# Performance work log

Hardware: AMD Instinct MI355X
Metric: run time of the kernel (lower is better)

Reference implementation:

```python
import jax, jax.numpy as jnp
import numpy as np

D_MODEL = 1024
NUM_HEADS = 16
D_K = D_MODEL // NUM_HEADS
SCALE = D_K ** 0.5


def setup_inputs() -> dict:
    key = jax.random.key(0)
    k1, k2, k3, k4, k5 = jax.random.split(key, 5)
    B, T = 4, 2048
    x = jax.random.normal(k1, (B, T, D_MODEL), dtype=jnp.float32)
    # torch nn.Linear: y = x @ W.T + b ; store W in (in, out) layout for jax
    s = 1.0 / np.sqrt(D_MODEL)
    w_qkv = jax.random.uniform(k2, (D_MODEL, 3 * D_MODEL), jnp.float32, -s, s)
    b_qkv = jax.random.uniform(k3, (3 * D_MODEL,), jnp.float32, -s, s)
    w_out = jax.random.uniform(k4, (D_MODEL, D_MODEL), jnp.float32, -s, s)
    b_out = jax.random.uniform(k5, (D_MODEL,), jnp.float32, -s, s)
    return {"x": x, "w_qkv": w_qkv, "b_qkv": b_qkv, "w_out": w_out, "b_out": b_out}


def reference(x, w_qkv, b_qkv, w_out, b_out):
    B, T, D = x.shape
    qkv = x @ w_qkv + b_qkv  # (B, T, 3D)
    q, k, v = jnp.split(qkv, 3, axis=-1)

    def split_heads(t):
        return t.reshape(B, T, NUM_HEADS, D_K).transpose(0, 2, 1, 3)  # (B,H,T,d_k)

    q, k, v = split_heads(q), split_heads(k), split_heads(v)
    scores = jnp.einsum("bhtd,bhsd->bhts", q, k) / SCALE  # (B,H,T,T)
    attn = jax.nn.softmax(scores, axis=-1)
    ctx = jnp.einsum("bhts,bhsd->bhtd", attn, v)  # (B,H,T,d_k)
    ctx = ctx.transpose(0, 2, 1, 3).reshape(B, T, D)
    y = ctx @ w_out + b_out
    return y
```

## Files before the change

### kernel.cpp

```cpp
#include <hip/hip_runtime.h>
#include <hip/hip_bf16.h>


using v8bf  = __attribute__((ext_vector_type(8))) __bf16;
using f32x4 = __attribute__((ext_vector_type(4))) float;
using f32x16 = __attribute__((ext_vector_type(16))) float;
typedef unsigned int uv2 __attribute__((ext_vector_type(2)));

__device__ __forceinline__ unsigned short f2bf(float f) {
  union { float f; unsigned int u; } v; v.f = f;
  unsigned int u = v.u;
  u += 0x7FFFu + ((u >> 16) & 1u);
  return (unsigned short)(u >> 16);
}

#if __has_builtin(__builtin_amdgcn_cvt_pk_bf16_f32)
__device__ __forceinline__ unsigned int pack2bf(float a, float b) {
  typedef __bf16 bf16x2 __attribute__((ext_vector_type(2)));
  bf16x2 r = __builtin_amdgcn_cvt_pk_bf16_f32(a, b);
  return __builtin_bit_cast(unsigned int, r);
}
#else
__device__ __forceinline__ unsigned int pack2bf(float a, float b) {
  return (unsigned int)f2bf(a) | ((unsigned int)f2bf(b) << 16);
}
#endif

__device__ __forceinline__ void async16(const void* g, void* l) {
  __builtin_amdgcn_global_load_lds(
      (__attribute__((address_space(1))) void*)g,
      (__attribute__((address_space(3))) void*)l, 16, 0, 0);
}

__global__ __launch_bounds__(256) void convert_bf16(const float* __restrict__ in,
                                                    unsigned short* __restrict__ out,
                                                    int n) {
  int i = (blockIdx.x * 256 + threadIdx.x) * 4;
  if (i < n) {
    float4 v = *(const float4*)(in + i);
    ushort4 o;
    o.x = f2bf(v.x); o.y = f2bf(v.y); o.z = f2bf(v.z); o.w = f2bf(v.w);
    *(ushort4*)(out + i) = o;
  }
}

__global__ __launch_bounds__(256) void transpose_bf16(const float* __restrict__ in,
                                                      unsigned short* __restrict__ out,
                                                      int K, int N) {
  __shared__ unsigned short tile[64][65];
  int k0 = blockIdx.x * 64, n0 = blockIdx.y * 64;
  for (int i = threadIdx.x; i < 4096; i += 256) {
    int r = i >> 6, c = i & 63;
    tile[r][c] = f2bf(in[(size_t)(k0 + r) * N + n0 + c]);
  }
  __syncthreads();
  for (int i = threadIdx.x; i < 4096; i += 256) {
    int r = i >> 6, c = i & 63;
    out[(size_t)(n0 + r) * K + k0 + c] = tile[c][r];
  }
}

__device__ __forceinline__ void gemm128(const unsigned short* __restrict__ A,
                                        const unsigned short* __restrict__ Bt,
                                        int m0, int n0,
                                        unsigned short* As, unsigned short* Bs,
                                        f32x4 acc[4][4]) {
  const int tid = threadIdx.x;
  const int w = tid >> 6, lane = tid & 63, quad = lane >> 4, l16 = lane & 15;
  const int wm = (w >> 1) * 64, wn = (w & 1) * 64;

  const int srow = w * 32 + (lane >> 3);
  const int cg = (lane & 7) ^ (lane >> 3);
  const size_t a_g = (size_t)(m0 + srow) * 1024 + cg * 8;
  const size_t b_g = (size_t)(n0 + srow) * 1024 + cg * 8;
  const int lds_off = srow * 64 + (lane & 7) * 8;

  const int l7 = l16 & 7;
  const int a_rd0 = (wm + l16) * 128 + ((quad ^ l7) << 4);
  const int a_rd1 = (wm + l16) * 128 + (((4 + quad) ^ l7) << 4);
  const int b_rd0 = (wn + l16) * 128 + ((quad ^ l7) << 4);
  const int b_rd1 = (wn + l16) * 128 + (((4 + quad) ^ l7) << 4);

  for (int k0 = 0; k0 < 1024; k0 += 64) {
#pragma unroll
    for (int j = 0; j < 4; j++) {
      async16(A + a_g + (size_t)j * 8192 + k0, As + lds_off + j * 512);
      async16(Bt + b_g + (size_t)j * 8192 + k0, Bs + lds_off + j * 512);
    }
    __syncthreads();
#pragma unroll
    for (int ks = 0; ks < 2; ks++) {
      v8bf af[4], bfr[4];
#pragma unroll
      for (int i = 0; i < 4; i++) {
        af[i]  = *(const v8bf*)((const char*)As + (ks ? a_rd1 : a_rd0) + i * 2048);
        bfr[i] = *(const v8bf*)((const char*)Bs + (ks ? b_rd1 : b_rd0) + i * 2048);
      }
#pragma unroll
      for (int i = 0; i < 4; i++)
#pragma unroll
        for (int jn = 0; jn < 4; jn++)
          acc[i][jn] = __builtin_amdgcn_mfma_f32_16x16x32_bf16(af[i], bfr[jn], acc[i][jn], 0, 0, 0);
    }
    __syncthreads();
  }
}

__global__ __launch_bounds__(256) void qkv_gemm(const unsigned short* __restrict__ xb,
                                                const unsigned short* __restrict__ wt,
                                                const float* __restrict__ bias,
                                                unsigned short* __restrict__ Q,
                                                unsigned short* __restrict__ K,
                                                unsigned short* __restrict__ VT) {
  __shared__ __align__(16) unsigned char pool[128 * 136 * 2];
  unsigned short* As = (unsigned short*)pool;
  unsigned short* Bs = (unsigned short*)(pool + 16384);
  unsigned short* Tr = (unsigned short*)pool;

  f32x4 acc[4][4];
#pragma unroll
  for (int i = 0; i < 4; i++)
#pragma unroll
    for (int j = 0; j < 4; j++) acc[i][j] = (f32x4){0.f, 0.f, 0.f, 0.f};

  const int m0 = blockIdx.x * 128, n0 = blockIdx.y * 128;
  gemm128(xb, wt, m0, n0, As, Bs, acc);

  const int tid = threadIdx.x;
  const int w = tid >> 6, lane = tid & 63, quad = lane >> 4, l16 = lane & 15;
  const int wm = (w >> 1) * 64, wn = (w & 1) * 64;
  const int seg = n0 >> 10;

  if (seg < 2) {
    const float sc = (seg == 0) ? 0.18033688011112042f : 1.0f;
    unsigned short* dst = (seg == 0) ? Q : K;
#pragma unroll
    for (int jn = 0; jn < 4; jn++) {
      const int n = n0 + wn + jn * 16 + l16;
      const float bv = bias[n];
      const int nn = n & 1023, h = nn >> 6, d = nn & 63;
#pragma unroll
      for (int i = 0; i < 4; i++) {
#pragma unroll
        for (int r = 0; r < 4; r++) {
          const int m = m0 + wm + i * 16 + quad * 4 + r;
          const int b_ = m >> 11, t = m & 2047;
          dst[(((size_t)(b_ * 16 + h)) * 2048 + t) * 64 + d] =
              f2bf((acc[i][jn][r] + bv) * sc);
        }
      }
    }
  } else {
    const int TP = 136;
#pragma unroll
    for (int jn = 0; jn < 4; jn++) {
      const int nl = wn + jn * 16 + l16;
      const float bv = bias[n0 + nl];
#pragma unroll
      for (int i = 0; i < 4; i++) {
        const int ml = wm + i * 16 + quad * 4;
        ushort4 v4;
        v4.x = f2bf(acc[i][jn][0] + bv);
        v4.y = f2bf(acc[i][jn][1] + bv);
        v4.z = f2bf(acc[i][jn][2] + bv);
        v4.w = f2bf(acc[i][jn][3] + bv);
        *(ushort4*)&Tr[nl * TP + ml] = v4;
      }
    }
    __syncthreads();
    const int rl = tid >> 1, cb = (tid & 1) * 64;
    const int h0 = (n0 & 1023) >> 6;
    const int h = h0 + (rl >> 6), d = rl & 63;
    const int b_ = m0 >> 11, t = m0 & 2047;
    unsigned short* dst = VT + (((size_t)(b_ * 16 + h)) * 64 + d) * 2048 + t + cb;
    const unsigned short* src = &Tr[rl * TP + cb];
#pragma unroll
    for (int c = 0; c < 8; c++)
      *(uint4*)(dst + c * 8) = *(const uint4*)(src + c * 8);
  }
}

__global__ __launch_bounds__(256, 2) void flash_attn(const unsigned short* __restrict__ Q,
                                                     const unsigned short* __restrict__ K,
                                                     const unsigned short* __restrict__ VT,
                                                     unsigned short* __restrict__ ctx) {
  const int bh    = blockIdx.x;
  const int qtile = blockIdx.y;
  const int tid = threadIdx.x;
  const int w = tid >> 6, lane = tid & 63, hi = lane >> 5, l32 = lane & 31;
  const int q0 = qtile * 256;

  const unsigned short* Qb = Q  + (size_t)bh * 2048 * 64;
  const unsigned short* Kb = K  + (size_t)bh * 2048 * 64;
  const unsigned short* Vb = VT + (size_t)bh * 64 * 2048;

  __shared__ __align__(16) unsigned short Ks[3 * 4096];
  __shared__ __align__(16) unsigned short Vs[3 * 4096];

  const int sr = w * 8 + (lane >> 3);
  const int cg = (lane & 7) ^ ((lane >> 3) & 7);
  const int lds_off = sr * 64 + (lane & 7) * 8;

  v8bf qf[2][4];
#pragma unroll
  for (int qt = 0; qt < 2; qt++) {
    const int qrow = q0 + w * 64 + qt * 32 + l32;
#pragma unroll
    for (int kc = 0; kc < 4; kc++)
      qf[qt][kc] = *(const v8bf*)(Qb + (size_t)qrow * 64 + kc * 16 + hi * 8);
  }

  f32x16 o[2][2];
  f32x16 st[2][2];
  float l_[2] = {0.f, 0.f};
#pragma unroll
  for (int qt = 0; qt < 2; qt++)
#pragma unroll
    for (int mt = 0; mt < 2; mt++)
#pragma unroll
      for (int r = 0; r < 16; r++) o[qt][mt][r] = 0.f;

  f32x16 fz;
#pragma unroll
  for (int r = 0; r < 16; r++) fz[r] = 0.f;

  auto stage = [&](int buf, int s0) {
    unsigned short* Kd = Ks + buf * 4096;
    unsigned short* Vd = Vs + buf * 4096;
#pragma unroll
    for (int j = 0; j < 2; j++) {
      async16(Kb + (size_t)(s0 + sr + j * 32) * 64 + cg * 8, Kd + lds_off + j * 2048);
      async16(Vb + (size_t)(sr + j * 32) * 2048 + s0 + cg * 8, Vd + lds_off + j * 2048);
    }
  };

  const int l7 = l32 & 7;

  auto computeS = [&](const unsigned short* Kc) {
#pragma unroll
    for (int sf = 0; sf < 2; sf++) {
      v8bf ak[4];
#pragma unroll
      for (int kc = 0; kc < 4; kc++)
        ak[kc] = *(const v8bf*)((const char*)Kc +
                   (sf * 32 + l32) * 128 + (((2 * kc + hi) ^ l7) << 4));
#pragma unroll
      for (int qt = 0; qt < 2; qt++) {
        f32x16 s = __builtin_amdgcn_mfma_f32_32x32x16_bf16(ak[0], qf[qt][0], fz, 0, 0, 0);
#pragma unroll
        for (int kc = 1; kc < 4; kc++)
          s = __builtin_amdgcn_mfma_f32_32x32x16_bf16(ak[kc], qf[qt][kc], s, 0, 0, 0);
        st[qt][sf] = s;
      }
    }
  };

  auto softmax_pack = [&](uint2 pk[2][2][4]) {
#pragma unroll
    for (int qt = 0; qt < 2; qt++) {
      float a = 0.f;
#pragma unroll
      for (int sf = 0; sf < 2; sf++)
#pragma unroll
        for (int r = 0; r < 16; r++) {
          const float pv = __builtin_amdgcn_exp2f(st[qt][sf][r]);
          st[qt][sf][r] = pv;
          a += pv;
        }
      l_[qt] += a;
#pragma unroll
      for (int sf = 0; sf < 2; sf++)
#pragma unroll
        for (int g = 0; g < 4; g++) {
          pk[qt][sf][g].x = pack2bf(st[qt][sf][g * 4 + 0], st[qt][sf][g * 4 + 1]);
          pk[qt][sf][g].y = pack2bf(st[qt][sf][g * 4 + 2], st[qt][sf][g * 4 + 3]);
        }
    }
  };

  auto pv = [&](const unsigned short* Vc, uint2 pk[2][2][4]) {
    v8bf vf[2][4];
#pragma unroll
    for (int mt = 0; mt < 2; mt++)
#pragma unroll
      for (int kc = 0; kc < 4; kc++)
        vf[mt][kc] = *(const v8bf*)((const char*)Vc +
                       (mt * 32 + l32) * 128 + (((2 * kc + hi) ^ l7) << 4));
#pragma unroll
    for (int qt = 0; qt < 2; qt++) {
#pragma unroll
      for (int kc = 0; kc < 4; kc++) {
        const int sf = kc >> 1, c2 = (kc & 1) * 2;
        const uint2 olo = pk[qt][sf][c2];
        const uint2 ohi = pk[qt][sf][c2 + 1];
        uint4 u;
#if __has_builtin(__builtin_amdgcn_permlane32_swap)
        uv2 rx = __builtin_amdgcn_permlane32_swap(olo.x, ohi.x, false, false);
        uv2 ry = __builtin_amdgcn_permlane32_swap(olo.y, ohi.y, false, false);
        u.x = rx[0]; u.y = ry[0]; u.z = rx[1]; u.w = ry[1];
#else
        uint2 send, recv;
        send.x = hi ? olo.x : ohi.x;
        send.y = hi ? olo.y : ohi.y;
        recv.x = __shfl_xor(send.x, 32, 64);
        recv.y = __shfl_xor(send.y, 32, 64);
        u.x = hi ? recv.x : olo.x;
        u.y = hi ? recv.y : olo.y;
        u.z = hi ? ohi.x : recv.x;
        u.w = hi ? ohi.y : recv.y;
#endif
        const v8bf pf = __builtin_bit_cast(v8bf, u);
#pragma unroll
        for (int mt = 0; mt < 2; mt++)
          o[qt][mt] = __builtin_amdgcn_mfma_f32_32x32x16_bf16(vf[mt][kc], pf, o[qt][mt], 0, 0, 0);
      }
    }
  };

  stage(0, 0);
  __syncthreads();
  stage(1, 64);
  computeS(Ks);

  int cs = 1, cp = 0, cn = 2;
  for (int it = 1; it < 32; ++it) {
    __syncthreads();
    if (it < 31) stage(cn, (it + 1) * 64);
    uint2 pk[2][2][4];
    softmax_pack(pk);
    computeS(Ks + cs * 4096);
    pv(Vs + cp * 4096, pk);
    const int t = cp; cp = cs; cs = cn; cn = t;
  }
  {
    uint2 pk[2][2][4];
    softmax_pack(pk);
    pv(Vs + cp * 4096, pk);
  }

  const int b_ = bh >> 4, h = bh & 15;
#pragma unroll
  for (int qt = 0; qt < 2; qt++) {
    float lt = l_[qt];
    lt += __shfl_xor(lt, 32, 64);
    const float inv = 1.0f / lt;
    const int t = q0 + w * 64 + qt * 32 + l32;
    unsigned short* cr = ctx + ((size_t)(b_ * 2048 + t)) * 1024 + h * 64;
#pragma unroll
    for (int mt = 0; mt < 2; mt++)
#pragma unroll
      for (int g = 0; g < 4; g++) {
        uint2 pkv;
        pkv.x = pack2bf(o[qt][mt][g * 4 + 0] * inv, o[qt][mt][g * 4 + 1] * inv);
        pkv.y = pack2bf(o[qt][mt][g * 4 + 2] * inv, o[qt][mt][g * 4 + 3] * inv);
        *(uint2*)(cr + mt * 32 + g * 8 + hi * 4) = pkv;
      }
  }
}

__global__ __launch_bounds__(256) void out_gemm(const unsigned short* __restrict__ ctx,
                                                const unsigned short* __restrict__ wt,
                                                const float* __restrict__ bias,
                                                float* __restrict__ out) {
  __shared__ __align__(16) unsigned short As[128 * 64];
  __shared__ __align__(16) unsigned short Bs[128 * 64];
  f32x4 acc[4][4];
#pragma unroll
  for (int i = 0; i < 4; i++)
#pragma unroll
    for (int j = 0; j < 4; j++) acc[i][j] = (f32x4){0.f, 0.f, 0.f, 0.f};

  const int m0 = blockIdx.x * 128, n0 = blockIdx.y * 128;
  gemm128(ctx, wt, m0, n0, As, Bs, acc);

  const int tid = threadIdx.x;
  const int w = tid >> 6, lane = tid & 63, quad = lane >> 4, l16 = lane & 15;
  const int wm = (w >> 1) * 64, wn = (w & 1) * 64;
#pragma unroll
  for (int jn = 0; jn < 4; jn++) {
    const int n = n0 + wn + jn * 16 + l16;
    const float bv = bias[n];
#pragma unroll
    for (int i = 0; i < 4; i++) {
#pragma unroll
      for (int r = 0; r < 4; r++) {
        const int m = m0 + wm + i * 16 + quad * 4 + r;
        out[(size_t)m * 1024 + n] = acc[i][jn][r] + bv;
      }
    }
  }
}

extern "C" void kernel_launch(void* const* d_in, const int* in_sizes, int n_in,
                              void* d_out, int out_size, void* d_ws, size_t ws_size,
                              hipStream_t stream) {
  const float* x     = (const float*)d_in[0];
  const float* w_qkv = (const float*)d_in[1];
  const float* b_qkv = (const float*)d_in[2];
  const float* w_out = (const float*)d_in[3];
  const float* b_out = (const float*)d_in[4];
  float* out = (float*)d_out;

  char* ws = (char*)d_ws;
  unsigned short* XB  = (unsigned short*)(ws + 0);
  unsigned short* WQT = (unsigned short*)(ws + 16777216);
  unsigned short* WOT = (unsigned short*)(ws + 23068672);
  unsigned short* Qp  = (unsigned short*)(ws + 25165824);
  unsigned short* Kp  = (unsigned short*)(ws + 41943040);
  unsigned short* VTp = (unsigned short*)(ws + 58720256);
  unsigned short* CTX = (unsigned short*)(ws + 75497472);

  convert_bf16<<<8192, 256, 0, stream>>>(x, XB, 8388608);
  transpose_bf16<<<dim3(16, 48), 256, 0, stream>>>(w_qkv, WQT, 1024, 3072);
  transpose_bf16<<<dim3(16, 16), 256, 0, stream>>>(w_out, WOT, 1024, 1024);
  qkv_gemm<<<dim3(64, 24), 256, 0, stream>>>(XB, WQT, b_qkv, Qp, Kp, VTp);
  flash_attn<<<dim3(64, 8), 256, 0, stream>>>(Qp, Kp, VTp, CTX);
  out_gemm<<<dim3(64, 8), 256, 0, stream>>>(CTX, WOT, b_out, out);
}
```

Measured before the change: 265.6 us.

## Halve flash-attention query tile per block to raise occupancy and block count

Each wave now handles 32 query rows instead of 64, so each block covers 128 queries and twice as many blocks are launched. Register arrays for the accumulators and scores are halved, and the launch bound is raised to 4 blocks per CU. K staging drops to double buffering while V keeps three buffers. The loop now runs PV before the next S computation, and V fragments are loaded from LDS inside the PV loop. The cost is that every K/V tile is reloaded from memory twice as often, since less reuse happens per block.

```diff
diff --git a/kernel.cpp b/kernel.cpp
--- a/kernel.cpp
+++ b/kernel.cpp
@@ -180,7 +180,7 @@
   }
 }
 
-__global__ __launch_bounds__(256, 2) void flash_attn(const unsigned short* __restrict__ Q,
+__global__ __launch_bounds__(256, 4) void flash_attn(const unsigned short* __restrict__ Q,
                                                      const unsigned short* __restrict__ K,
                                                      const unsigned short* __restrict__ VT,
                                                      unsigned short* __restrict__ ctx) {
@@ -188,50 +188,46 @@
   const int qtile = blockIdx.y;
   const int tid = threadIdx.x;
   const int w = tid >> 6, lane = tid & 63, hi = lane >> 5, l32 = lane & 31;
-  const int q0 = qtile * 256;
+  const int q0 = qtile * 128;
 
   const unsigned short* Qb = Q  + (size_t)bh * 2048 * 64;
   const unsigned short* Kb = K  + (size_t)bh * 2048 * 64;
   const unsigned short* Vb = VT + (size_t)bh * 64 * 2048;
 
-  __shared__ __align__(16) unsigned short Ks[3 * 4096];
+  __shared__ __align__(16) unsigned short Ks[2 * 4096];
   __shared__ __align__(16) unsigned short Vs[3 * 4096];
 
   const int sr = w * 8 + (lane >> 3);
   const int cg = (lane & 7) ^ ((lane >> 3) & 7);
   const int lds_off = sr * 64 + (lane & 7) * 8;
 
-  v8bf qf[2][4];
-#pragma unroll
-  for (int qt = 0; qt < 2; qt++) {
-    const int qrow = q0 + w * 64 + qt * 32 + l32;
+  v8bf qf[4];
+  {
+    const int qrow = q0 + w * 32 + l32;
 #pragma unroll
     for (int kc = 0; kc < 4; kc++)
-      qf[qt][kc] = *(const v8bf*)(Qb + (size_t)qrow * 64 + kc * 16 + hi * 8);
-  }
-
-  f32x16 o[2][2];
-  f32x16 st[2][2];
-  float l_[2] = {0.f, 0.f};
-#pragma unroll
-  for (int qt = 0; qt < 2; qt++)
-#pragma unroll
-    for (int mt = 0; mt < 2; mt++)
-#pragma unroll
-      for (int r = 0; r < 16; r++) o[qt][mt][r] = 0.f;
-
-  f32x16 fz;
-#pragma unroll
-  for (int r = 0; r < 16; r++) fz[r] = 0.f;
-
-  auto stage = [&](int buf, int s0) {
+      qf[kc] = *(const v8bf*)(Qb + (size_t)qrow * 64 + kc * 16 + hi * 8);
+  }
+
+  f32x16 o[2];
+  f32x16 st[2];
+  float l_ = 0.f;
+#pragma unroll
+  for (int mt = 0; mt < 2; mt++)
+#pragma unroll
+    for (int r = 0; r < 16; r++) o[mt][r] = 0.f;
+
+  auto stageK = [&](int buf, int s0) {
     unsigned short* Kd = Ks + buf * 4096;
+#pragma unroll
+    for (int j = 0; j < 2; j++)
+      async16(Kb + (size_t)(s0 + sr + j * 32) * 64 + cg * 8, Kd + lds_off + j * 2048);
+  };
+  auto stageV = [&](int buf, int s0) {
     unsigned short* Vd = Vs + buf * 4096;
 #pragma unroll
-    for (int j = 0; j < 2; j++) {
-      async16(Kb + (size_t)(s0 + sr + j * 32) * 64 + cg * 8, Kd + lds_off + j * 2048);
+    for (int j = 0; j < 2; j++)
       async16(Vb + (size_t)(sr + j * 32) * 2048 + s0 + cg * 8, Vd + lds_off + j * 2048);
-    }
   };
 
   const int l7 = l32 & 7;
@@ -244,115 +240,94 @@
       for (int kc = 0; kc < 4; kc++)
         ak[kc] = *(const v8bf*)((const char*)Kc +
                    (sf * 32 + l32) * 128 + (((2 * kc + hi) ^ l7) << 4));
-#pragma unroll
-      for (int qt = 0; qt < 2; qt++) {
-        f32x16 s = __builtin_amdgcn_mfma_f32_32x32x16_bf16(ak[0], qf[qt][0], fz, 0, 0, 0);
-#pragma unroll
-        for (int kc = 1; kc < 4; kc++)
-          s = __builtin_amdgcn_mfma_f32_32x32x16_bf16(ak[kc], qf[qt][kc], s, 0, 0, 0);
-        st[qt][sf] = s;
-      }
-    }
-  };
-
-  auto softmax_pack = [&](uint2 pk[2][2][4]) {
-#pragma unroll
-    for (int qt = 0; qt < 2; qt++) {
-      float a = 0.f;
-#pragma unroll
-      for (int sf = 0; sf < 2; sf++)
-#pragma unroll
-        for (int r = 0; r < 16; r++) {
-          const float pv = __builtin_amdgcn_exp2f(st[qt][sf][r]);
-          st[qt][sf][r] = pv;
-          a += pv;
-        }
-      l_[qt] += a;
-#pragma unroll
-      for (int sf = 0; sf < 2; sf++)
-#pragma unroll
-        for (int g = 0; g < 4; g++) {
-          pk[qt][sf][g].x = pack2bf(st[qt][sf][g * 4 + 0], st[qt][sf][g * 4 + 1]);
-          pk[qt][sf][g].y = pack2bf(st[qt][sf][g * 4 + 2], st[qt][sf][g * 4 + 3]);
-        }
-    }
-  };
-
-  auto pv = [&](const unsigned short* Vc, uint2 pk[2][2][4]) {
-    v8bf vf[2][4];
-#pragma unroll
-    for (int mt = 0; mt < 2; mt++)
-#pragma unroll
-      for (int kc = 0; kc < 4; kc++)
-        vf[mt][kc] = *(const v8bf*)((const char*)Vc +
-                       (mt * 32 + l32) * 128 + (((2 * kc + hi) ^ l7) << 4));
-#pragma unroll
-    for (int qt = 0; qt < 2; qt++) {
-#pragma unroll
-      for (int kc = 0; kc < 4; kc++) {
-        const int sf = kc >> 1, c2 = (kc & 1) * 2;
-        const uint2 olo = pk[qt][sf][c2];
-        const uint2 ohi = pk[qt][sf][c2 + 1];
-        uint4 u;
+      f32x16 s = __builtin_amdgcn_mfma_f32_32x32x16_bf16(ak[0], qf[0], (f32x16)(0.f), 0, 0, 0);
+#pragma unroll
+      for (int kc = 1; kc < 4; kc++)
+        s = __builtin_amdgcn_mfma_f32_32x32x16_bf16(ak[kc], qf[kc], s, 0, 0, 0);
+      st[sf] = s;
+    }
+  };
+
+  auto softmax = [&]() {
+    float a0 = 0.f, a1 = 0.f;
+#pragma unroll
+    for (int sf = 0; sf < 2; sf++)
+#pragma unroll
+      for (int r = 0; r < 16; r++) {
+        const float pv = __builtin_amdgcn_exp2f(st[sf][r]);
+        st[sf][r] = pv;
+        if (r & 1) a1 += pv; else a0 += pv;
+      }
+    l_ += a0 + a1;
+  };
+
+  auto pv = [&](const unsigned short* Vc) {
+#pragma unroll
+    for (int kc = 0; kc < 4; kc++) {
+      const int sf = kc >> 1, e0 = (kc & 1) * 8;
+      uint2 olo, ohi;
+      olo.x = pack2bf(st[sf][e0 + 0], st[sf][e0 + 1]);
+      olo.y = pack2bf(st[sf][e0 + 2], st[sf][e0 + 3]);
+      ohi.x = pack2bf(st[sf][e0 + 4], st[sf][e0 + 5]);
+      ohi.y = pack2bf(st[sf][e0 + 6], st[sf][e0 + 7]);
+      uint4 u;
 #if __has_builtin(__builtin_amdgcn_permlane32_swap)
-        uv2 rx = __builtin_amdgcn_permlane32_swap(olo.x, ohi.x, false, false);
-        uv2 ry = __builtin_amdgcn_permlane32_swap(olo.y, ohi.y, false, false);
-        u.x = rx[0]; u.y = ry[0]; u.z = rx[1]; u.w = ry[1];
+      uv2 rx = __builtin_amdgcn_permlane32_swap(olo.x, ohi.x, false, false);
+      uv2 ry = __builtin_amdgcn_permlane32_swap(olo.y, ohi.y, false, false);
+      u.x = rx[0]; u.y = ry[0]; u.z = rx[1]; u.w = ry[1];
 #else
-        uint2 send, recv;
-        send.x = hi ? olo.x : ohi.x;
-        send.y = hi ? olo.y : ohi.y;
-        recv.x = __shfl_xor(send.x, 32, 64);
-        recv.y = __shfl_xor(send.y, 32, 64);
-        u.x = hi ? recv.x : olo.x;
-        u.y = hi ? recv.y : olo.y;
-        u.z = hi ? ohi.x : recv.x;
-        u.w = hi ? ohi.y : recv.y;
+      uint2 send, recv;
+      send.x = hi ? olo.x : ohi.x;
+      send.y = hi ? olo.y : ohi.y;
+      recv.x = __shfl_xor(send.x, 32, 64);
+      recv.y = __shfl_xor(send.y, 32, 64);
+      u.x = hi ? recv.x : olo.x;
+      u.y = hi ? recv.y : olo.y;
+      u.z = hi ? ohi.x : recv.x;
+      u.w = hi ? ohi.y : recv.y;
 #endif
-        const v8bf pf = __builtin_bit_cast(v8bf, u);
-#pragma unroll
-        for (int mt = 0; mt < 2; mt++)
-          o[qt][mt] = __builtin_amdgcn_mfma_f32_32x32x16_bf16(vf[mt][kc], pf, o[qt][mt], 0, 0, 0);
-      }
-    }
-  };
-
-  stage(0, 0);
+      const v8bf pf = __builtin_bit_cast(v8bf, u);
+#pragma unroll
+      for (int mt = 0; mt < 2; mt++) {
+        const v8bf vfm = *(const v8bf*)((const char*)Vc +
+                           (mt * 32 + l32) * 128 + (((2 * kc + hi) ^ l7) << 4));
+        o[mt] = __builtin_amdgcn_mfma_f32_32x32x16_bf16(vfm, pf, o[mt], 0, 0, 0);
+      }
+    }
+  };
+
+  stageK(0, 0); stageV(0, 0);
   __syncthreads();
-  stage(1, 64);
+  stageK(1, 64); stageV(1, 64);
   computeS(Ks);
 
-  int cs = 1, cp = 0, cn = 2;
+  int vp = 0, vn = 2;
   for (int it = 1; it < 32; ++it) {
     __syncthreads();
-    if (it < 31) stage(cn, (it + 1) * 64);
-    uint2 pk[2][2][4];
-    softmax_pack(pk);
-    computeS(Ks + cs * 4096);
-    pv(Vs + cp * 4096, pk);
-    const int t = cp; cp = cs; cs = cn; cn = t;
-  }
+    if (it < 31) { stageK((it + 1) & 1, (it + 1) * 64); stageV(vn, (it + 1) * 64); }
+    softmax();
+    pv(Vs + vp * 4096);
+    computeS(Ks + (it & 1) * 4096);
+    vp = (vp == 2) ? 0 : vp + 1;
+    vn = (vn == 2) ? 0 : vn + 1;
+  }
+  softmax();
+  pv(Vs + vp * 4096);
+
+  const int b_ = bh >> 4, h = bh & 15;
   {
-    uint2 pk[2][2][4];
-    softmax_pack(pk);
-    pv(Vs + cp * 4096, pk);
-  }
-
-  const int b_ = bh >> 4, h = bh & 15;
-#pragma unroll
-  for (int qt = 0; qt < 2; qt++) {
-    float lt = l_[qt];
+    float lt = l_;
     lt += __shfl_xor(lt, 32, 64);
     const float inv = 1.0f / lt;
-    const int t = q0 + w * 64 + qt * 32 + l32;
+    const int t = q0 + w * 32 + l32;
     unsigned short* cr = ctx + ((size_t)(b_ * 2048 + t)) * 1024 + h * 64;
 #pragma unroll
     for (int mt = 0; mt < 2; mt++)
 #pragma unroll
       for (int g = 0; g < 4; g++) {
         uint2 pkv;
-        pkv.x = pack2bf(o[qt][mt][g * 4 + 0] * inv, o[qt][mt][g * 4 + 1] * inv);
-        pkv.y = pack2bf(o[qt][mt][g * 4 + 2] * inv, o[qt][mt][g * 4 + 3] * inv);
+        pkv.x = pack2bf(o[mt][g * 4 + 0] * inv, o[mt][g * 4 + 1] * inv);
+        pkv.y = pack2bf(o[mt][g * 4 + 2] * inv, o[mt][g * 4 + 3] * inv);
         *(uint2*)(cr + mt * 32 + g * 8 + hi * 4) = pkv;
       }
   }
@@ -414,6 +389,6 @@
   transpose_bf16<<<dim3(16, 48), 256, 0, stream>>>(w_qkv, WQT, 1024, 3072);
   transpose_bf16<<<dim3(16, 16), 256, 0, stream>>>(w_out, WOT, 1024, 1024);
   qkv_gemm<<<dim3(64, 24), 256, 0, stream>>>(XB, WQT, b_qkv, Qp, Kp, VTp);
-  flash_attn<<<dim3(64, 8), 256, 0, stream>>>(Qp, Kp, VTp, CTX);
+  flash_attn<<<dim3(64, 16), 256, 0, stream>>>(Qp, Kp, VTp, CTX);
   out_gemm<<<dim3(64, 8), 256, 0, stream>>>(CTX, WOT, b_out, out);
 }
```

After: 276.5 us. 4.1% more time.

## Use 256x128 triple-buffered pipelined GEMM tiles with block swizzle for projections

Applied to the files above, without the earlier changes.

Replaces the single-buffered 128x128 GEMM core with a 256x128 tile over 512 threads. Global-to-LDS async copies now run through a three-stage ring, gated by explicit vmcnt waits, so the next tiles load while MFMAs execute. The loop also adds s_setprio around the MFMA bursts and remaps block indices so blocks sharing a weight column-tile run close together for L2 reuse. The cost is about 144KB of LDS per block, which limits each CU to one resident block. The hand-written wait counts and barriers must also stay in step with the number of copies each stage issues.

```diff
diff --git a/kernel.cpp b/kernel.cpp
--- a/kernel.cpp
+++ b/kernel.cpp
@@ -60,7 +60,43 @@
   }
 }
 
-__device__ __forceinline__ void gemm128(const unsigned short* __restrict__ A,
+#define GKSTEP(VMSTR, CUR, DOSTAGE, KNEXT)                                     \
+  {                                                                            \
+    asm volatile("s_waitcnt vmcnt(" VMSTR ")" ::: "memory");                   \
+    __builtin_amdgcn_s_barrier();                                              \
+    __builtin_amdgcn_sched_barrier(0);                                         \
+    const unsigned short* Ab = As + (CUR) * 16384;                             \
+    const unsigned short* Bb = Bs + (CUR) * 8192;                              \
+    v8bf a0[4], b0[4], a1[4], b1[4];                                           \
+    _Pragma("unroll") for (int i_ = 0; i_ < 4; i_++) {                         \
+      a0[i_] = *(const v8bf*)((const char*)Ab + (wm + i_ * 16 + l16) * 128 +   \
+                              ((quad ^ l7) << 4));                             \
+      b0[i_] = *(const v8bf*)((const char*)Bb + (wn + i_ * 16 + l16) * 128 +   \
+                              ((quad ^ l7) << 4));                             \
+      a1[i_] = *(const v8bf*)((const char*)Ab + (wm + i_ * 16 + l16) * 128 +   \
+                              (((4 + quad) ^ l7) << 4));                       \
+      b1[i_] = *(const v8bf*)((const char*)Bb + (wn + i_ * 16 + l16) * 128 +   \
+                              (((4 + quad) ^ l7) << 4));                       \
+    }                                                                          \
+    __builtin_amdgcn_s_setprio(1);                                             \
+    _Pragma("unroll") for (int i_ = 0; i_ < 4; i_++)                           \
+      _Pragma("unroll") for (int j_ = 0; j_ < 4; j_++)                         \
+        acc[i_][j_] = __builtin_amdgcn_mfma_f32_16x16x32_bf16(                 \
+            a0[i_], b0[j_], acc[i_][j_], 0, 0, 0);                             \
+    __builtin_amdgcn_s_setprio(0);                                             \
+    asm volatile("s_waitcnt lgkmcnt(0)" ::: "memory");                         \
+    __builtin_amdgcn_s_barrier();                                              \
+    __builtin_amdgcn_sched_barrier(0);                                         \
+    if (DOSTAGE) stage((CUR), (KNEXT));                                        \
+    __builtin_amdgcn_s_setprio(1);                                             \
+    _Pragma("unroll") for (int i_ = 0; i_ < 4; i_++)                           \
+      _Pragma("unroll") for (int j_ = 0; j_ < 4; j_++)                         \
+        acc[i_][j_] = __builtin_amdgcn_mfma_f32_16x16x32_bf16(                 \
+            a1[i_], b1[j_], acc[i_][j_], 0, 0, 0);                             \
+    __builtin_amdgcn_s_setprio(0);                                             \
+  }
+
+__device__ __forceinline__ void gemm256(const unsigned short* __restrict__ A,
                                         const unsigned short* __restrict__ Bt,
                                         int m0, int n0,
                                         unsigned short* As, unsigned short* Bs,
@@ -68,53 +104,46 @@
   const int tid = threadIdx.x;
   const int w = tid >> 6, lane = tid & 63, quad = lane >> 4, l16 = lane & 15;
   const int wm = (w >> 1) * 64, wn = (w & 1) * 64;
-
-  const int srow = w * 32 + (lane >> 3);
-  const int cg = (lane & 7) ^ (lane >> 3);
-  const size_t a_g = (size_t)(m0 + srow) * 1024 + cg * 8;
-  const size_t b_g = (size_t)(n0 + srow) * 1024 + cg * 8;
-  const int lds_off = srow * 64 + (lane & 7) * 8;
-
   const int l7 = l16 & 7;
-  const int a_rd0 = (wm + l16) * 128 + ((quad ^ l7) << 4);
-  const int a_rd1 = (wm + l16) * 128 + (((4 + quad) ^ l7) << 4);
-  const int b_rd0 = (wn + l16) * 128 + ((quad ^ l7) << 4);
-  const int b_rd1 = (wn + l16) * 128 + (((4 + quad) ^ l7) << 4);
-
-  for (int k0 = 0; k0 < 1024; k0 += 64) {
-#pragma unroll
-    for (int j = 0; j < 4; j++) {
-      async16(A + a_g + (size_t)j * 8192 + k0, As + lds_off + j * 512);
-      async16(Bt + b_g + (size_t)j * 8192 + k0, Bs + lds_off + j * 512);
-    }
-    __syncthreads();
-#pragma unroll
-    for (int ks = 0; ks < 2; ks++) {
-      v8bf af[4], bfr[4];
-#pragma unroll
-      for (int i = 0; i < 4; i++) {
-        af[i]  = *(const v8bf*)((const char*)As + (ks ? a_rd1 : a_rd0) + i * 2048);
-        bfr[i] = *(const v8bf*)((const char*)Bs + (ks ? b_rd1 : b_rd0) + i * 2048);
-      }
-#pragma unroll
-      for (int i = 0; i < 4; i++)
-#pragma unroll
-        for (int jn = 0; jn < 4; jn++)
-          acc[i][jn] = __builtin_amdgcn_mfma_f32_16x16x32_bf16(af[i], bfr[jn], acc[i][jn], 0, 0, 0);
-    }
-    __syncthreads();
-  }
-}
-
-__global__ __launch_bounds__(256) void qkv_gemm(const unsigned short* __restrict__ xb,
-                                                const unsigned short* __restrict__ wt,
-                                                const float* __restrict__ bias,
-                                                unsigned short* __restrict__ Q,
-                                                unsigned short* __restrict__ K,
-                                                unsigned short* __restrict__ VT) {
-  __shared__ __align__(16) unsigned char pool[128 * 136 * 2];
+
+  const int row8 = tid >> 3;
+  const int cg = (tid & 7) ^ (row8 & 7);
+  const int lds8 = row8 * 64 + (tid & 7) * 8;
+
+  auto stage = [&](int buf, int k0) {
+    unsigned short* Ad = As + buf * 16384;
+    unsigned short* Bd = Bs + buf * 8192;
+#pragma unroll
+    for (int j = 0; j < 4; j++)
+      async16(A + (size_t)(m0 + row8 + j * 64) * 1024 + k0 + cg * 8,
+              Ad + lds8 + j * 4096);
+#pragma unroll
+    for (int j = 0; j < 2; j++)
+      async16(Bt + (size_t)(n0 + row8 + j * 64) * 1024 + k0 + cg * 8,
+              Bd + lds8 + j * 4096);
+  };
+
+  stage(0, 0); stage(1, 64); stage(2, 128);
+
+  int cur = 0;
+  for (int t = 0; t < 14; ++t) {
+    GKSTEP("12", cur, (t < 13), (t + 3) * 64);
+    cur = (cur == 2) ? 0 : cur + 1;
+  }
+  GKSTEP("6", cur, false, 0);
+  cur = (cur == 2) ? 0 : cur + 1;
+  GKSTEP("0", cur, false, 0);
+}
+
+__global__ __launch_bounds__(512, 2) void qkv_gemm(const unsigned short* __restrict__ xb,
+                                                   const unsigned short* __restrict__ wt,
+                                                   const float* __restrict__ bias,
+                                                   unsigned short* __restrict__ Q,
+                                                   unsigned short* __restrict__ K,
+                                                   unsigned short* __restrict__ VT) {
+  __shared__ __align__(16) unsigned char pool[147456];
   unsigned short* As = (unsigned short*)pool;
-  unsigned short* Bs = (unsigned short*)(pool + 16384);
+  unsigned short* Bs = (unsigned short*)(pool + 98304);
   unsigned short* Tr = (unsigned short*)pool;
 
   f32x4 acc[4][4];
@@ -123,8 +152,10 @@
 #pragma unroll
     for (int j = 0; j < 4; j++) acc[i][j] = (f32x4){0.f, 0.f, 0.f, 0.f};
 
-  const int m0 = blockIdx.x * 128, n0 = blockIdx.y * 128;
-  gemm128(xb, wt, m0, n0, As, Bs, acc);
+  const int id = blockIdx.x;
+  const int swz = (id & 7) * 96 + (id >> 3);
+  const int m0 = (swz & 31) * 256, n0 = (swz >> 5) * 128;
+  gemm256(xb, wt, m0, n0, As, Bs, acc);
 
   const int tid = threadIdx.x;
   const int w = tid >> 6, lane = tid & 63, quad = lane >> 4, l16 = lane & 15;
@@ -151,7 +182,7 @@
       }
     }
   } else {
-    const int TP = 136;
+    const int TP = 264;
 #pragma unroll
     for (int jn = 0; jn < 4; jn++) {
       const int nl = wn + jn * 16 + l16;
@@ -168,11 +199,11 @@
       }
     }
     __syncthreads();
-    const int rl = tid >> 1, cb = (tid & 1) * 64;
+    const int rl = tid >> 2, cb = (tid & 3) * 64;
     const int h0 = (n0 & 1023) >> 6;
     const int h = h0 + (rl >> 6), d = rl & 63;
-    const int b_ = m0 >> 11, t = m0 & 2047;
-    unsigned short* dst = VT + (((size_t)(b_ * 16 + h)) * 64 + d) * 2048 + t + cb;
+    const int b_ = m0 >> 11, t0 = m0 & 2047;
+    unsigned short* dst = VT + (((size_t)(b_ * 16 + h)) * 64 + d) * 2048 + t0 + cb;
     const unsigned short* src = &Tr[rl * TP + cb];
 #pragma unroll
     for (int c = 0; c < 8; c++)
@@ -358,20 +389,24 @@
   }
 }
 
-__global__ __launch_bounds__(256) void out_gemm(const unsigned short* __restrict__ ctx,
-                                                const unsigned short* __restrict__ wt,
-                                                const float* __restrict__ bias,
-                                                float* __restrict__ out) {
-  __shared__ __align__(16) unsigned short As[128 * 64];
-  __shared__ __align__(16) unsigned short Bs[128 * 64];
+__global__ __launch_bounds__(512, 2) void out_gemm(const unsigned short* __restrict__ ctx,
+                                                   const unsigned short* __restrict__ wt,
+                                                   const float* __restrict__ bias,
+                                                   float* __restrict__ out) {
+  __shared__ __align__(16) unsigned char pool[147456];
+  unsigned short* As = (unsigned short*)pool;
+  unsigned short* Bs = (unsigned short*)(pool + 98304);
+
   f32x4 acc[4][4];
 #pragma unroll
   for (int i = 0; i < 4; i++)
 #pragma unroll
     for (int j = 0; j < 4; j++) acc[i][j] = (f32x4){0.f, 0.f, 0.f, 0.f};
 
-  const int m0 = blockIdx.x * 128, n0 = blockIdx.y * 128;
-  gemm128(ctx, wt, m0, n0, As, Bs, acc);
+  const int id = blockIdx.x;
+  const int swz = (id & 7) * 32 + (id >> 3);
+  const int m0 = (swz & 31) * 256, n0 = (swz >> 5) * 128;
+  gemm256(ctx, wt, m0, n0, As, Bs, acc);
 
   const int tid = threadIdx.x;
   const int w = tid >> 6, lane = tid & 63, quad = lane >> 4, l16 = lane & 15;
@@ -413,7 +448,7 @@
   convert_bf16<<<8192, 256, 0, stream>>>(x, XB, 8388608);
   transpose_bf16<<<dim3(16, 48), 256, 0, stream>>>(w_qkv, WQT, 1024, 3072);
   transpose_bf16<<<dim3(16, 16), 256, 0, stream>>>(w_out, WOT, 1024, 1024);
-  qkv_gemm<<<dim3(64, 24), 256, 0, stream>>>(XB, WQT, b_qkv, Qp, Kp, VTp);
+  qkv_gemm<<<768, 512, 0, stream>>>(XB, WQT, b_qkv, Qp, Kp, VTp);
   flash_attn<<<dim3(64, 8), 256, 0, stream>>>(Qp, Kp, VTp, CTX);
-  out_gemm<<<dim3(64, 8), 256, 0, stream>>>(CTX, WOT, b_out, out);
-}
+  out_gemm<<<256, 512, 0, stream>>>(CTX, WOT, b_out, out);
+}
```

Result: slower. 290.2 us (+9.3%).
